# Kernel tuning notes

Hardware: AMD Instinct MI355X
Metric: run time of the kernel (lower is better)

## Reference

```python
import jax, jax.numpy as jnp
import numpy as np

WS = 8        # window_size
SHIFT = 4     # shift_size
NH = 6        # num_heads
EPS = 1e-5


def _rel_pos_index(ws):
    coords = np.stack(np.meshgrid(np.arange(ws), np.arange(ws), indexing='ij'))  # [2,ws,ws]
    cf = coords.reshape(2, -1)                      # [2, ws*ws]
    rel = cf[:, :, None] - cf[:, None, :]           # [2, N, N]
    rel = rel.transpose(1, 2, 0)                    # [N, N, 2]
    rel[:, :, 0] += ws - 1
    rel[:, :, 1] += ws - 1
    rel[:, :, 0] *= 2 * ws - 1
    return rel.sum(-1)                              # [N, N] int


def _attn_mask(H, W, ws, shift):
    img = np.zeros((H, W), dtype=np.float32)
    slices = (slice(0, -ws), slice(-ws, -shift), slice(-shift, None))
    cnt = 0
    for hs in slices:
        for wsl in slices:
            img[hs, wsl] = cnt
            cnt += 1
    mw = img.reshape(H // ws, ws, W // ws, ws).transpose(0, 2, 1, 3).reshape(-1, ws * ws)
    diff = mw[:, None, :] - mw[:, :, None]          # [nW, N, N]
    return np.where(diff != 0, -100.0, 0.0).astype(np.float32)


def _layernorm(x, g, b):
    mu = x.mean(-1, keepdims=True)
    var = ((x - mu) ** 2).mean(-1, keepdims=True)
    return (x - mu) * jax.lax.rsqrt(var + EPS) * g + b


def setup_inputs() -> dict:
    key = jax.random.key(0)
    ks = jax.random.split(key, 8)
    C, HID = 192, 768
    return {
        'x': jax.random.normal(ks[0], (8, 128, 128, C), jnp.float32),
        'g1': jnp.ones((C,), jnp.float32),
        'b1': jnp.zeros((C,), jnp.float32),
        'qkv_w': jax.random.normal(ks[1], (3 * C, C), jnp.float32) * 0.02,
        'qkv_b': jnp.zeros((3 * C,), jnp.float32),
        'rpb_table': jax.random.normal(ks[2], ((2 * WS - 1) ** 2, NH), jnp.float32) * 0.02,
        'proj_w': jax.random.normal(ks[3], (C, C), jnp.float32) * 0.02,
        'proj_b': jnp.zeros((C,), jnp.float32),
        'g2': jnp.ones((C,), jnp.float32),
        'b2': jnp.zeros((C,), jnp.float32),
        'fc1_w': jax.random.normal(ks[4], (HID, C), jnp.float32) * 0.02,
        'fc1_b': jnp.zeros((HID,), jnp.float32),
        'fc2_w': jax.random.normal(ks[5], (C, HID), jnp.float32) * 0.02,
        'fc2_b': jnp.zeros((C,), jnp.float32),
    }


def reference(x, g1, b1, qkv_w, qkv_b, rpb_table, proj_w, proj_b, g2, b2,
              fc1_w, fc1_b, fc2_w, fc2_b):
    B, H, W, C = x.shape
    N = WS * WS
    hd = C // NH
    scale = hd ** -0.5

    rpi = jnp.asarray(_rel_pos_index(WS))                 # [N,N] static
    mask = jnp.asarray(_attn_mask(H, W, WS, SHIFT))       # [nW,N,N] static
    nW = mask.shape[0]

    shortcut = x.reshape(B, H * W, C)
    xn = _layernorm(shortcut, g1, b1).reshape(B, H, W, C)

    # cyclic shift
    xs = jnp.roll(xn, shift=(-SHIFT, -SHIFT), axis=(1, 2))

    # window partition -> [B*nW, N, C]
    win = xs.reshape(B, H // WS, WS, W // WS, WS, C).transpose(0, 1, 3, 2, 4, 5)
    win = win.reshape(-1, N, C)
    B_ = win.shape[0]

    # qkv
    qkv = jnp.einsum('bnc,oc->bno', win, qkv_w) + qkv_b   # [B_,N,3C]
    qkv = qkv.reshape(B_, N, 3, NH, hd).transpose(2, 0, 3, 1, 4)  # [3,B_,NH,N,hd]
    q, k, v = qkv[0] * scale, qkv[1], qkv[2]

    attn = jnp.einsum('bhnd,bhmd->bhnm', q, k)            # [B_,NH,N,N]
    bias = rpb_table[rpi.reshape(-1)].reshape(N, N, NH).transpose(2, 0, 1)
    attn = attn + bias[None]
    attn = attn.reshape(B, nW, NH, N, N) + mask[None, :, None]
    attn = jax.nn.softmax(attn.reshape(B_, NH, N, N), axis=-1)

    out = jnp.einsum('bhnm,bhmd->bhnd', attn, v)          # [B_,NH,N,hd]
    out = out.transpose(0, 2, 1, 3).reshape(B_, N, C)
    out = jnp.einsum('bnc,oc->bno', out, proj_w) + proj_b

    # window reverse -> [B,H,W,C]
    out = out.reshape(B, H // WS, W // WS, WS, WS, C).transpose(0, 1, 3, 2, 4, 5)
    out = out.reshape(B, H, W, C)
    out = jnp.roll(out, shift=(SHIFT, SHIFT), axis=(1, 2)).reshape(B, H * W, C)

    x1 = shortcut + out
    h = _layernorm(x1, g2, b2)
    h = jnp.einsum('bnc,hc->bnh', h, fc1_w) + fc1_b
    h = jax.nn.gelu(h, approximate=False)
    h = jnp.einsum('bnh,ch->bnc', h, fc2_w) + fc2_b
    x2 = x1 + h
    return x2.reshape(B, H, W, C)
```

## Files before the change

kernel.cpp:

```cpp
#include <hip/hip_runtime.h>
#include <hip/hip_bf16.h>

typedef __attribute__((ext_vector_type(8))) short s16x8;
typedef __attribute__((ext_vector_type(4))) float f32x4;

__device__ __forceinline__ unsigned short f2bf(float f){
    __hip_bfloat16 h = __float2bfloat16(f);
    return *reinterpret_cast<unsigned short*>(&h);
}

__device__ __forceinline__ int flab(int g){ return (g < 120) ? 0 : ((g < 124) ? 1 : 2); }

__device__ __forceinline__ void async16(const void* g, void* l){
    __builtin_amdgcn_global_load_lds(
        (const __attribute__((address_space(1))) unsigned int*)g,
        (__attribute__((address_space(3))) unsigned int*)l, 16, 0, 0);
}

__global__ __launch_bounds__(256) void wconv_all(
    const float* __restrict__ w0, const float* __restrict__ w1,
    const float* __restrict__ w2, const float* __restrict__ w3,
    unsigned short* __restrict__ o0, unsigned short* __restrict__ o1,
    unsigned short* __restrict__ o2, unsigned short* __restrict__ o3)
{
    int i = blockIdx.x*256 + threadIdx.x;
    if (i < 110592) o0[i] = f2bf(w0[i]);
    if (i < 36864)  o1[i] = f2bf(w1[i]);
    if (i < 147456) o2[i] = f2bf(w2[i]);
    if (i < 147456) o3[i] = f2bf(w3[i]);
}

__global__ __launch_bounds__(256) void lnqkv_kernel(
    const float* __restrict__ x, const float* __restrict__ g1, const float* __restrict__ b1,
    const unsigned short* __restrict__ wq, const float* __restrict__ qkvb,
    unsigned short* __restrict__ qo, unsigned short* __restrict__ ko,
    unsigned short* __restrict__ vo)
{
    __shared__ __attribute__((aligned(16))) unsigned short win[64*200];
    __shared__ __attribute__((aligned(16))) unsigned short Bs[64*200];
    const int b_ = blockIdx.x;
    const int bb = b_>>8, wi = b_&255, wh = wi>>4, ww = wi&15;
    const int tid = threadIdx.x;
    const int wv = tid>>6, lane = tid&63, lrow = lane&15, quad = lane>>4;

    {
        const int n = tid>>2, q4 = tid&3;
        const int r = n>>3, c = n&7;
        const int hh = (wh*8 + r + 4)&127, wp = (ww*8 + c + 4)&127;
        const float* px = x + (((size_t)bb*128+hh)*128+wp)*192 + q4*48;
        float v[48];
        #pragma unroll
        for (int m=0;m<12;++m) *(float4*)(v+m*4) = *(const float4*)(px+m*4);
        float s = 0.f;
        #pragma unroll
        for (int k=0;k<48;++k) s += v[k];
        s += __shfl_xor(s,1); s += __shfl_xor(s,2);
        float mu = s*(1.0f/192.0f);
        float qv = 0.f;
        #pragma unroll
        for (int k=0;k<48;++k){ float d=v[k]-mu; qv += d*d; }
        qv += __shfl_xor(qv,1); qv += __shfl_xor(qv,2);
        float rstd = rsqrtf(qv*(1.0f/192.0f) + 1e-5f);
        const float* pg = g1 + q4*48;
        const float* pb = b1 + q4*48;
        unsigned short* pw = win + n*200 + q4*48;
        #pragma unroll
        for (int k=0;k<48;++k) pw[k] = f2bf((v[k]-mu)*rstd*pg[k] + pb[k]);
    }
    __syncthreads();

    s16x8 af[6];
    #pragma unroll
    for (int kc=0;kc<6;++kc)
        af[kc] = *(const s16x8*)(win + (wv*16+lrow)*200 + kc*32 + quad*8);

    for (int ot=0; ot<9; ++ot) {
        const int o0 = ot*64;
        __syncthreads();
        #pragma unroll
        for (int t=0;t<6;++t) {
            int cid = tid + t*256;
            *(int4*)(Bs + (cid/24)*200 + (cid%24)*8) =
                *(const int4*)(wq + (size_t)o0*192 + cid*8);
        }
        __syncthreads();
        f32x4 acc[4];
        #pragma unroll
        for (int j=0;j<4;++j) acc[j] = (f32x4){0.f,0.f,0.f,0.f};
        #pragma unroll
        for (int kc=0;kc<6;++kc)
            #pragma unroll
            for (int j=0;j<4;++j) {
                s16x8 bf = *(const s16x8*)(Bs + (j*16+lrow)*200 + kc*32 + quad*8);
                acc[j] = __builtin_amdgcn_mfma_f32_16x16x32_bf16(af[kc], bf, acc[j], 0, 0, 0);
            }
        __syncthreads();
        unsigned short* T = Bs;
        const int part = ot/3;
        float bv[4];
        #pragma unroll
        for (int j=0;j<4;++j) bv[j] = qkvb[o0 + j*16 + lrow];

        if (part < 2) {
            const float scale = (part==0) ? 0.17677669529663687f : 1.0f;
            #pragma unroll
            for (int j=0;j<4;++j)
                #pragma unroll
                for (int rg=0;rg<4;++rg) {
                    int n2 = wv*16 + quad*4 + rg;
                    T[n2*72 + j*16 + lrow] = f2bf((acc[j][rg]+bv[j])*scale);
                }
            __syncthreads();
            unsigned short* dst = (part==0) ? qo : ko;
            #pragma unroll
            for (int t=0;t<2;++t) {
                int c = tid + t*256;
                int n2 = c>>3, blk = c&7;
                int o_in = o0 + blk*8 - part*192;
                int head = o_in>>5, d = o_in&31;
                *(int4*)(dst + (((size_t)b_*6+head)*64 + n2)*32 + d) =
                    *(const int4*)(T + n2*72 + blk*8);
            }
        } else {
            #pragma unroll
            for (int j=0;j<4;++j)
                #pragma unroll
                for (int rg=0;rg<4;++rg) {
                    int n2 = wv*16 + quad*4 + rg;
                    T[(j*16+lrow)*72 + n2] = f2bf(acc[j][rg]+bv[j]);
                }
            __syncthreads();
            #pragma unroll
            for (int t=0;t<2;++t) {
                int c = tid + t*256;
                int ol = c>>3, nb = (c&7)*8;
                int o_in = o0 + ol - 384;
                int head = o_in>>5, d = o_in&31;
                *(int4*)(vo + (((size_t)b_*6+head)*32 + d)*64 + nb) =
                    *(const int4*)(T + ol*72 + nb);
            }
        }
    }
}

__global__ __launch_bounds__(384) void attn_kernel(
    const unsigned short* __restrict__ q, const unsigned short* __restrict__ k,
    const unsigned short* __restrict__ vT, const float* __restrict__ rpb,
    unsigned short* __restrict__ ao)
{
    __shared__ float rpb_s[1350];
    __shared__ __attribute__((aligned(16))) unsigned short p_lds[6*4608];
    const int b_ = blockIdx.x;
    const int h = threadIdx.x >> 6;
    const int lane = threadIdx.x & 63, lrow = lane & 15, quad = lane >> 4;
    for (int i = threadIdx.x; i < 1350; i += 384) rpb_s[i] = rpb[i];
    __syncthreads();

    const size_t hb = ((size_t)b_*6 + h)*2048;
    const unsigned short* qb = q  + hb;
    const unsigned short* kb = k  + hb;
    const unsigned short* vb = vT + hb;

    s16x8 qf[4], kf[4];
    #pragma unroll
    for (int i = 0; i < 4; ++i) qf[i] = *(const s16x8*)(qb + (i*16+lrow)*32 + quad*8);
    #pragma unroll
    for (int j = 0; j < 4; ++j) kf[j] = *(const s16x8*)(kb + (j*16+lrow)*32 + quad*8);

    const f32x4 zz = {0.f,0.f,0.f,0.f};
    f32x4 s[4][4];
    #pragma unroll
    for (int i = 0; i < 4; ++i)
        #pragma unroll
        for (int j = 0; j < 4; ++j)
            s[i][j] = __builtin_amdgcn_mfma_f32_16x16x32_bf16(qf[i], kf[j], zz, 0, 0, 0);

    const int wi = b_ & 255, wh = wi >> 4, ww = wi & 15;
    int labm[4];
    #pragma unroll
    for (int j = 0; j < 4; ++j) {
        int m = j*16 + lrow;
        labm[j] = flab(wh*8 + (m >> 3))*3 + flab(ww*8 + (m & 7));
    }
    unsigned short* pl = p_lds + h*4608;
    #pragma unroll
    for (int i = 0; i < 4; ++i) {
        #pragma unroll
        for (int rg = 0; rg < 4; ++rg) {
            int n = i*16 + quad*4 + rg;
            int rn = n >> 3, cn = n & 7;
            int labn = flab(wh*8 + rn)*3 + flab(ww*8 + cn);
            float vals[4];
            float vmax = -1e30f;
            #pragma unroll
            for (int j = 0; j < 4; ++j) {
                int m = j*16 + lrow;
                int idx = ((rn - (m >> 3) + 7)*15 + (cn - (m & 7) + 7))*6 + h;
                float val = s[i][j][rg] + rpb_s[idx];
                if (labn != labm[j]) val -= 100.f;
                vals[j] = val;
                vmax = fmaxf(vmax, val);
            }
            #pragma unroll
            for (int o = 1; o < 16; o <<= 1) vmax = fmaxf(vmax, __shfl_xor(vmax, o));
            float sum = 0.f;
            #pragma unroll
            for (int j = 0; j < 4; ++j) { vals[j] = __expf(vals[j] - vmax); sum += vals[j]; }
            #pragma unroll
            for (int o = 1; o < 16; o <<= 1) sum += __shfl_xor(sum, o);
            float inv = 1.f / sum;
            #pragma unroll
            for (int j = 0; j < 4; ++j) pl[n*72 + j*16 + lrow] = f2bf(vals[j]*inv);
        }
    }
    __syncthreads();

    f32x4 oacc[4][2];
    #pragma unroll
    for (int i = 0; i < 4; ++i) { oacc[i][0] = zz; oacc[i][1] = zz; }
    #pragma unroll
    for (int kc = 0; kc < 2; ++kc) {
        s16x8 vf[2];
        #pragma unroll
        for (int jd = 0; jd < 2; ++jd)
            vf[jd] = *(const s16x8*)(vb + (jd*16+lrow)*64 + kc*32 + quad*8);
        #pragma unroll
        for (int i = 0; i < 4; ++i) {
            s16x8 pf = *(const s16x8*)(pl + (i*16+lrow)*72 + kc*32 + quad*8);
            #pragma unroll
            for (int jd = 0; jd < 2; ++jd)
                oacc[i][jd] = __builtin_amdgcn_mfma_f32_16x16x32_bf16(pf, vf[jd], oacc[i][jd], 0, 0, 0);
        }
    }
    unsigned short* ob = ao + (size_t)b_*12288 + h*32;
    #pragma unroll
    for (int i = 0; i < 4; ++i)
        #pragma unroll
        for (int jd = 0; jd < 2; ++jd)
            #pragma unroll
            for (int rg = 0; rg < 4; ++rg) {
                int n = i*16 + quad*4 + rg;
                ob[(size_t)n*192 + jd*16 + lrow] = f2bf(oacc[i][jd][rg]);
            }
}

__device__ __forceinline__ void mm64x192(
    const unsigned short* __restrict__ A, const unsigned short* __restrict__ W,
    size_t m0, unsigned short* As, unsigned short* Bs, f32x4 (&acc)[12])
{
    const int tid = threadIdx.x, wv = tid>>6, lane = tid&63;
    const int lrow = lane&15, quad = lane>>4;
    const int grow = lane>>2;
    const int gcb  = (lane&3) ^ ((lane>>3)&3);
    #pragma unroll
    for (int j=0;j<12;++j) acc[j] = (f32x4){0.f,0.f,0.f,0.f};

    const unsigned short* Ab = A + (m0 + grow)*192 + gcb*8;
    const unsigned short* Wb = W + (size_t)grow*192 + gcb*8;

    auto issue = [&](int k0, unsigned short* Ad, unsigned short* Bd) {
        async16(Ab + (size_t)(wv*16)*192 + k0,     Ad + wv*512);
        async16(Wb + (size_t)(wv*16)*192 + k0,     Bd + wv*512);
        async16(Wb + (size_t)((wv+4)*16)*192 + k0, Bd + (wv+4)*512);
        async16(Wb + (size_t)((wv+8)*16)*192 + k0, Bd + (wv+8)*512);
    };
    issue(0, As, Bs);
    int cur = 0;
    for (int k0=0; k0<192; k0+=32) {
        __syncthreads();
        if (k0+32 < 192) issue(k0+32, As + (cur^1)*2048, Bs + (cur^1)*6144);
        const unsigned short* Ac = As + cur*2048;
        const unsigned short* Bc = Bs + cur*6144;
        const int rs = (quad ^ ((lrow>>1)&3)) << 3;
        s16x8 af = *(const s16x8*)(Ac + (wv*16+lrow)*32 + rs);
        #pragma unroll
        for (int j=0;j<12;++j) {
            s16x8 bf = *(const s16x8*)(Bc + (j*16+lrow)*32 + rs);
            acc[j] = __builtin_amdgcn_mfma_f32_16x16x32_bf16(af, bf, acc[j], 0, 0, 0);
        }
        cur ^= 1;
    }
}

__global__ __launch_bounds__(256) void projln_kernel(
    const unsigned short* __restrict__ A, const unsigned short* __restrict__ W,
    const float* __restrict__ pbias, const float* __restrict__ x,
    const float* __restrict__ g2, const float* __restrict__ b2,
    float* __restrict__ x1, unsigned short* __restrict__ xln2b)
{
    __shared__ __attribute__((aligned(16))) char smem[32768];
    unsigned short* As = (unsigned short*)smem;
    unsigned short* Bs = (unsigned short*)(smem + 8192);
    const int b_ = blockIdx.x;
    const int tid = threadIdx.x, wv = tid>>6, lane = tid&63;
    const int lrow = lane&15, quad = lane>>4;
    const size_t m0 = (size_t)b_*64;

    f32x4 acc[12];
    mm64x192(A, W, m0, As, Bs, acc);
    __syncthreads();

    const int bb = b_>>8, wi = b_&255, wh = wi>>4, ww = wi&15;
    float bv[12], gv[12], b2v[12];
    #pragma unroll
    for (int j=0;j<12;++j) {
        bv[j]  = pbias[j*16+lrow];
        gv[j]  = g2[j*16+lrow];
        b2v[j] = b2[j*16+lrow];
    }
    unsigned short* T = (unsigned short*)smem;
    #pragma unroll
    for (int rg=0;rg<4;++rg) {
        int n2 = wv*16 + quad*4 + rg;
        int r = n2>>3, c = n2&7;
        int hh = (wh*8+r+4)&127, wp = (ww*8+c+4)&127;
        size_t tok = ((size_t)bb*128+hh)*128 + wp;
        float xv[12];
        float s = 0.f;
        #pragma unroll
        for (int j=0;j<12;++j) {
            float t = acc[j][rg] + bv[j] + x[tok*192 + j*16 + lrow];
            xv[j] = t; s += t;
        }
        #pragma unroll
        for (int o=1;o<16;o<<=1) s += __shfl_xor(s, o);
        float mu = s*(1.0f/192.0f);
        float qv = 0.f;
        #pragma unroll
        for (int j=0;j<12;++j){ float d = xv[j]-mu; qv += d*d; }
        #pragma unroll
        for (int o=1;o<16;o<<=1) qv += __shfl_xor(qv, o);
        float rstd = rsqrtf(qv*(1.0f/192.0f) + 1e-5f);
        #pragma unroll
        for (int j=0;j<12;++j) {
            x1[tok*192 + j*16 + lrow] = xv[j];
            T[n2*200 + j*16 + lrow] = f2bf((xv[j]-mu)*rstd*gv[j] + b2v[j]);
        }
    }
    __syncthreads();
    #pragma unroll
    for (int t=0;t<6;++t) {
        int cid = tid + t*256;
        int n2 = cid/24, blk = cid%24;
        int r = n2>>3, c = n2&7;
        int hh = (wh*8+r+4)&127, wp = (ww*8+c+4)&127;
        size_t tok = ((size_t)bb*128+hh)*128 + wp;
        int row = (int)(tok & 127);
        int ks = blk>>2, kb = blk&3;
        int sw = (kb ^ ((row>>1)&3)) << 3;
        *(int4*)(xln2b + (tok>>7)*24576 + ks*4096 + row*32 + sw) =
            *(const int4*)(T + n2*200 + blk*8);
    }
}

__global__ __launch_bounds__(256, 4) void gemm_fc1_kernel(
    const unsigned short* __restrict__ Ablk, const unsigned short* __restrict__ Wm,
    const float* __restrict__ bias, unsigned short* __restrict__ h1b)
{
    __shared__ __attribute__((aligned(16))) char smem[28672];
    unsigned short* As = (unsigned short*)smem;
    unsigned short* Bs = (unsigned short*)(smem + 16384);
    const int bid = blockIdx.x;
    const int virt = (bid & 7)*1024 + (bid >> 3);
    const int mt = virt >> 3;
    const int o0 = (virt & 7)*96;
    const int tid = threadIdx.x, wv = tid>>6, lane = tid&63;
    const int lrow = lane&15, quad = lane>>4;
    const int grow = lane>>2, gcb = (lane&3)^((lane>>3)&3);

    const unsigned short* Asrc = Ablk + (size_t)mt*24576 + lane*8;
    const unsigned short* Wb = Wm + (size_t)(o0 + grow)*192 + gcb*8;

    f32x4 acc[2][6];
    #pragma unroll
    for (int i=0;i<2;++i)
        #pragma unroll
        for (int j=0;j<6;++j) acc[i][j] = (f32x4){0.f,0.f,0.f,0.f};

    auto issue = [&](int ks, unsigned short* Ad, unsigned short* Bd) {
        async16(Asrc + ks*4096 + wv*512,     Ad + wv*512);
        async16(Asrc + ks*4096 + (wv+4)*512, Ad + (wv+4)*512);
        async16(Wb + (size_t)(wv*16)*192 + ks*32, Bd + wv*512);
        if (wv < 2)
            async16(Wb + (size_t)((wv+4)*16)*192 + ks*32, Bd + (wv+4)*512);
    };
    issue(0, As, Bs);
    int cur = 0;
    for (int ks=0; ks<6; ++ks) {
        __syncthreads();
        if (ks < 5) issue(ks+1, As + (cur^1)*4096, Bs + (cur^1)*3072);
        const unsigned short* Ac = As + cur*4096;
        const unsigned short* Bc = Bs + cur*3072;
        const int rs = (quad ^ ((lrow>>1)&3)) << 3;
        s16x8 af[2], bf[6];
        #pragma unroll
        for (int i=0;i<2;++i)
            af[i] = *(const s16x8*)(Ac + (wv*32 + i*16 + lrow)*32 + rs);
        #pragma unroll
        for (int j=0;j<6;++j)
            bf[j] = *(const s16x8*)(Bc + (j*16 + lrow)*32 + rs);
        #pragma unroll
        for (int i=0;i<2;++i)
            #pragma unroll
            for (int j=0;j<6;++j)
                acc[i][j] = __builtin_amdgcn_mfma_f32_16x16x32_bf16(af[i], bf[j], acc[i][j], 0, 0, 0);
        cur ^= 1;
    }

    float bv[6];
    #pragma unroll
    for (int j=0;j<6;++j) bv[j] = bias[o0 + j*16 + lrow];
    __syncthreads();
    unsigned short* T = (unsigned short*)smem;
    #pragma unroll
    for (int i=0;i<2;++i)
        #pragma unroll
        for (int j=0;j<6;++j)
            #pragma unroll
            for (int rg=0;rg<4;++rg) {
                int ml = wv*32 + i*16 + quad*4 + rg;
                float v = acc[i][j][rg] + bv[j];
                float v2 = v*v;
                float z = v*(1.5957691216057308f + 0.07135481627f*v2);
                float r = v * __builtin_amdgcn_rcpf(1.f + __expf(-z));
                T[ml*104 + j*16 + lrow] = f2bf(r);
            }
    __syncthreads();
    unsigned short* hb = h1b + (size_t)mt*98304 + (o0>>5)*4096;
    #pragma unroll
    for (int t=0;t<6;++t) {
        int c = tid + t*256;
        int row = c/12, blk = c%12;
        int ks = blk>>2, kb = blk&3;
        int sw = (kb ^ ((row>>1)&3)) << 3;
        *(int4*)(hb + ks*4096 + row*32 + sw) = *(const int4*)(T + row*104 + blk*8);
    }
}

__global__ __launch_bounds__(256, 3) void gemm_fc2_kernel(
    const unsigned short* __restrict__ Ablk, const unsigned short* __restrict__ Wm,
    const float* __restrict__ bias, const float* __restrict__ x1, float* __restrict__ out)
{
    __shared__ __attribute__((aligned(16))) char smem[40960];
    unsigned short* As = (unsigned short*)smem;
    unsigned short* Bs = (unsigned short*)(smem + 16384);
    const int bid = blockIdx.x;
    const int virt = (bid & 7)*128 + (bid >> 3);
    const size_t m0 = (size_t)virt*128;
    const int tid = threadIdx.x, wv = tid>>6, lane = tid&63;
    const int lrow = lane&15, quad = lane>>4;
    const int grow = lane>>2, gcb = (lane&3)^((lane>>3)&3);

    const unsigned short* Asrc = Ablk + (size_t)virt*98304 + lane*8;
    const unsigned short* Wb = Wm + (size_t)grow*768 + gcb*8;

    f32x4 acc[2][12];
    #pragma unroll
    for (int i=0;i<2;++i)
        #pragma unroll
        for (int j=0;j<12;++j) acc[i][j] = (f32x4){0.f,0.f,0.f,0.f};

    auto issue = [&](int ks, unsigned short* Ad, unsigned short* Bd) {
        async16(Asrc + ks*4096 + wv*512,     Ad + wv*512);
        async16(Asrc + ks*4096 + (wv+4)*512, Ad + (wv+4)*512);
        #pragma unroll
        for (int it=0;it<3;++it) {
            int seg = wv + it*4;
            async16(Wb + (size_t)(seg*16)*768 + ks*32, Bd + seg*512);
        }
    };
    issue(0, As, Bs);
    int cur = 0;
    for (int ks=0; ks<24; ++ks) {
        __syncthreads();
        if (ks < 23) issue(ks+1, As + (cur^1)*4096, Bs + (cur^1)*6144);
        const unsigned short* Ac = As + cur*4096;
        const unsigned short* Bc = Bs + cur*6144;
        const int rs = (quad ^ ((lrow>>1)&3)) << 3;
        s16x8 af[2], bf[12];
        #pragma unroll
        for (int i=0;i<2;++i)
            af[i] = *(const s16x8*)(Ac + (wv*32 + i*16 + lrow)*32 + rs);
        #pragma unroll
        for (int j=0;j<12;++j)
            bf[j] = *(const s16x8*)(Bc + (j*16 + lrow)*32 + rs);
        #pragma unroll
        for (int i=0;i<2;++i)
            #pragma unroll
            for (int j=0;j<12;++j)
                acc[i][j] = __builtin_amdgcn_mfma_f32_16x16x32_bf16(af[i], bf[j], acc[i][j], 0, 0, 0);
        cur ^= 1;
    }

    float bv[12];
    #pragma unroll
    for (int j=0;j<12;++j) bv[j] = bias[j*16 + lrow];
    #pragma unroll
    for (int i=0;i<2;++i)
        #pragma unroll
        for (int j=0;j<12;++j)
            #pragma unroll
            for (int rg=0;rg<4;++rg) {
                size_t ad = (m0 + wv*32 + i*16 + quad*4 + rg)*192 + j*16 + lrow;
                out[ad] = acc[i][j][rg] + bv[j] + x1[ad];
            }
}

extern "C" void kernel_launch(void* const* d_in, const int* in_sizes, int n_in,
                              void* d_out, int out_size, void* d_ws, size_t ws_size,
                              hipStream_t stream)
{
    const float* x      = (const float*)d_in[0];
    const float* g1     = (const float*)d_in[1];
    const float* b1     = (const float*)d_in[2];
    const float* qkv_w  = (const float*)d_in[3];
    const float* qkv_b  = (const float*)d_in[4];
    const float* rpb    = (const float*)d_in[5];
    const float* proj_w = (const float*)d_in[6];
    const float* proj_b = (const float*)d_in[7];
    const float* g2     = (const float*)d_in[8];
    const float* b2     = (const float*)d_in[9];
    const float* fc1_w  = (const float*)d_in[10];
    const float* fc1_b  = (const float*)d_in[11];
    const float* fc2_w  = (const float*)d_in[12];
    const float* fc2_b  = (const float*)d_in[13];
    float* out = (float*)d_out;
    char* ws = (char*)d_ws;

    if (ws_size < 353206272ULL) return;

    unsigned short* qbuf  = (unsigned short*)(ws + 0);
    unsigned short* kbuf  = (unsigned short*)(ws + 50331648);
    unsigned short* vbuf  = (unsigned short*)(ws + 100663296);
    unsigned short* attnO = (unsigned short*)(ws + 150994944);
    float*          x1    = (float*)        (ws + 201326592);
    unsigned short* xln2  = (unsigned short*)(ws + 301989888);
    unsigned short* wq    = (unsigned short*)(ws + 352321536);
    unsigned short* wp    = (unsigned short*)(ws + 352321536 + 221184);
    unsigned short* w1    = (unsigned short*)(ws + 352321536 + 221184 + 73728);
    unsigned short* w2    = (unsigned short*)(ws + 352321536 + 221184 + 73728 + 294912);
    unsigned short* h1    = (unsigned short*)(ws + 0);

    wconv_all<<<576, 256, 0, stream>>>(qkv_w, proj_w, fc1_w, fc2_w, wq, wp, w1, w2);
    lnqkv_kernel<<<2048, 256, 0, stream>>>(x, g1, b1, wq, qkv_b, qbuf, kbuf, vbuf);
    attn_kernel<<<2048, 384, 0, stream>>>(qbuf, kbuf, vbuf, rpb, attnO);
    projln_kernel<<<2048, 256, 0, stream>>>(attnO, wp, proj_b, x, g2, b2, x1, xln2);
    gemm_fc1_kernel<<<8192, 256, 0, stream>>>(xln2, w1, fc1_b, h1);
    gemm_fc2_kernel<<<1024, 256, 0, stream>>>(h1, w2, fc2_b, x1, out);
}
```

Before: 575.6 us.

## Fuse fc1, GELU and fc2 into one MLP kernel keeping hidden activations in LDS

Replaces the separate fc1 and fc2 GEMM kernels with a single kernel in which each 512-thread block handles 64 tokens. The block computes fc1 plus GELU into a 96 KB LDS buffer and then runs fc2 from LDS, so the 768-wide hidden tensor never makes a round trip through global memory. The weight conversion now writes fc1/fc2 weights in a pre-tiled blocked layout so B fragments can be read straight from global memory (L2) without LDS staging. The trade-offs are the large LDS footprint, which limits occupancy, and weight reads that are now unpipelined global loads inside the MFMA loops.

```diff
diff --git a/kernel.cpp b/kernel.cpp
--- a/kernel.cpp
+++ b/kernel.cpp
@@ -26,8 +26,16 @@
     int i = blockIdx.x*256 + threadIdx.x;
     if (i < 110592) o0[i] = f2bf(w0[i]);
     if (i < 36864)  o1[i] = f2bf(w1[i]);
-    if (i < 147456) o2[i] = f2bf(w2[i]);
-    if (i < 147456) o3[i] = f2bf(w3[i]);
+    if (i < 147456) {
+        int o = i/192, k = i - o*192;
+        int oc = o/96, r = o - oc*96, ks = k>>5, c = k&31;
+        o2[((oc*6 + ks)*96 + r)*32 + c] = f2bf(w2[i]);
+    }
+    if (i < 147456) {
+        int o = i/768, k = i - o*768;
+        int q = o/48, r = o - q*48, ks = k>>5, c = k&31;
+        o3[((q*24 + ks)*48 + r)*32 + c] = f2bf(w3[i]);
+    }
 }
 
 __global__ __launch_bounds__(256) void lnqkv_kernel(
@@ -353,157 +361,112 @@
     }
 }
 
-__global__ __launch_bounds__(256, 4) void gemm_fc1_kernel(
-    const unsigned short* __restrict__ Ablk, const unsigned short* __restrict__ Wm,
-    const float* __restrict__ bias, unsigned short* __restrict__ h1b)
-{
-    __shared__ __attribute__((aligned(16))) char smem[28672];
-    unsigned short* As = (unsigned short*)smem;
-    unsigned short* Bs = (unsigned short*)(smem + 16384);
-    const int bid = blockIdx.x;
-    const int virt = (bid & 7)*1024 + (bid >> 3);
-    const int mt = virt >> 3;
-    const int o0 = (virt & 7)*96;
+__global__ __launch_bounds__(512, 2) void mlp_kernel(
+    const unsigned short* __restrict__ Ablk,
+    const unsigned short* __restrict__ W1b,
+    const float* __restrict__ fc1b,
+    const unsigned short* __restrict__ W2b,
+    const float* __restrict__ fc2b,
+    const float* __restrict__ x1, float* __restrict__ out)
+{
+    __shared__ __attribute__((aligned(16))) unsigned short Ald[6*2048];
+    __shared__ __attribute__((aligned(16))) unsigned short Hld[24*2048];
+    const int b_ = blockIdx.x;
+    const int mt = b_>>1, half = b_&1;
     const int tid = threadIdx.x, wv = tid>>6, lane = tid&63;
     const int lrow = lane&15, quad = lane>>4;
-    const int grow = lane>>2, gcb = (lane&3)^((lane>>3)&3);
-
-    const unsigned short* Asrc = Ablk + (size_t)mt*24576 + lane*8;
-    const unsigned short* Wb = Wm + (size_t)(o0 + grow)*192 + gcb*8;
-
-    f32x4 acc[2][6];
-    #pragma unroll
-    for (int i=0;i<2;++i)
+    const int rs = (quad ^ ((lrow>>1)&3)) << 3;
+
+    {
+        const unsigned short* src = Ablk + (size_t)mt*24576 + half*2048 + lane*8;
+        #pragma unroll
+        for (int r=0;r<3;++r) {
+            int c = r*8 + wv;
+            async16(src + (c>>2)*4096 + (c&3)*512, Ald + c*512);
+        }
+    }
+    __syncthreads();
+
+    f32x4 acc[4][6];
+    #pragma unroll
+    for (int i=0;i<4;++i)
         #pragma unroll
         for (int j=0;j<6;++j) acc[i][j] = (f32x4){0.f,0.f,0.f,0.f};
-
-    auto issue = [&](int ks, unsigned short* Ad, unsigned short* Bd) {
-        async16(Asrc + ks*4096 + wv*512,     Ad + wv*512);
-        async16(Asrc + ks*4096 + (wv+4)*512, Ad + (wv+4)*512);
-        async16(Wb + (size_t)(wv*16)*192 + ks*32, Bd + wv*512);
-        if (wv < 2)
-            async16(Wb + (size_t)((wv+4)*16)*192 + ks*32, Bd + (wv+4)*512);
-    };
-    issue(0, As, Bs);
-    int cur = 0;
-    for (int ks=0; ks<6; ++ks) {
-        __syncthreads();
-        if (ks < 5) issue(ks+1, As + (cur^1)*4096, Bs + (cur^1)*3072);
-        const unsigned short* Ac = As + cur*4096;
-        const unsigned short* Bc = Bs + cur*3072;
-        const int rs = (quad ^ ((lrow>>1)&3)) << 3;
-        s16x8 af[2], bf[6];
-        #pragma unroll
-        for (int i=0;i<2;++i)
-            af[i] = *(const s16x8*)(Ac + (wv*32 + i*16 + lrow)*32 + rs);
+    #pragma unroll 2
+    for (int ks=0;ks<6;++ks) {
+        s16x8 af[4], bf[6];
+        #pragma unroll
+        for (int i=0;i<4;++i)
+            af[i] = *(const s16x8*)(Ald + ks*2048 + (i*16+lrow)*32 + rs);
         #pragma unroll
         for (int j=0;j<6;++j)
-            bf[j] = *(const s16x8*)(Bc + (j*16 + lrow)*32 + rs);
-        #pragma unroll
-        for (int i=0;i<2;++i)
+            bf[j] = *(const s16x8*)(W1b + (size_t)((wv*6+ks)*96 + j*16+lrow)*32 + quad*8);
+        #pragma unroll
+        for (int i=0;i<4;++i)
             #pragma unroll
             for (int j=0;j<6;++j)
                 acc[i][j] = __builtin_amdgcn_mfma_f32_16x16x32_bf16(af[i], bf[j], acc[i][j], 0, 0, 0);
-        cur ^= 1;
-    }
-
-    float bv[6];
-    #pragma unroll
-    for (int j=0;j<6;++j) bv[j] = bias[o0 + j*16 + lrow];
-    __syncthreads();
-    unsigned short* T = (unsigned short*)smem;
+    }
+
+    {
+        float bv1[6];
+        #pragma unroll
+        for (int j=0;j<6;++j) bv1[j] = fc1b[wv*96 + j*16 + lrow];
+        #pragma unroll
+        for (int i=0;i<4;++i)
+            #pragma unroll
+            for (int j=0;j<6;++j)
+                #pragma unroll
+                for (int rg=0;rg<4;++rg) {
+                    int row = i*16 + quad*4 + rg;
+                    int o = wv*96 + j*16 + lrow;
+                    float v = acc[i][j][rg] + bv1[j];
+                    float v2 = v*v;
+                    float z = v*(1.5957691216057308f + 0.07135481627f*v2);
+                    float r = v * __builtin_amdgcn_rcpf(1.f + __expf(-z));
+                    int ksh = o>>5, c5 = o&31;
+                    Hld[ksh*2048 + row*32 + (((c5>>3) ^ ((row>>1)&3))<<3) + (c5&7)] = f2bf(r);
+                }
+    }
+    __syncthreads();
+
+    const int r0 = (wv>>2)*32, c0 = (wv&3)*48;
+    f32x4 a2[2][3];
     #pragma unroll
     for (int i=0;i<2;++i)
         #pragma unroll
-        for (int j=0;j<6;++j)
-            #pragma unroll
-            for (int rg=0;rg<4;++rg) {
-                int ml = wv*32 + i*16 + quad*4 + rg;
-                float v = acc[i][j][rg] + bv[j];
-                float v2 = v*v;
-                float z = v*(1.5957691216057308f + 0.07135481627f*v2);
-                float r = v * __builtin_amdgcn_rcpf(1.f + __expf(-z));
-                T[ml*104 + j*16 + lrow] = f2bf(r);
-            }
-    __syncthreads();
-    unsigned short* hb = h1b + (size_t)mt*98304 + (o0>>5)*4096;
-    #pragma unroll
-    for (int t=0;t<6;++t) {
-        int c = tid + t*256;
-        int row = c/12, blk = c%12;
-        int ks = blk>>2, kb = blk&3;
-        int sw = (kb ^ ((row>>1)&3)) << 3;
-        *(int4*)(hb + ks*4096 + row*32 + sw) = *(const int4*)(T + row*104 + blk*8);
-    }
-}
-
-__global__ __launch_bounds__(256, 3) void gemm_fc2_kernel(
-    const unsigned short* __restrict__ Ablk, const unsigned short* __restrict__ Wm,
-    const float* __restrict__ bias, const float* __restrict__ x1, float* __restrict__ out)
-{
-    __shared__ __attribute__((aligned(16))) char smem[40960];
-    unsigned short* As = (unsigned short*)smem;
-    unsigned short* Bs = (unsigned short*)(smem + 16384);
-    const int bid = blockIdx.x;
-    const int virt = (bid & 7)*128 + (bid >> 3);
-    const size_t m0 = (size_t)virt*128;
-    const int tid = threadIdx.x, wv = tid>>6, lane = tid&63;
-    const int lrow = lane&15, quad = lane>>4;
-    const int grow = lane>>2, gcb = (lane&3)^((lane>>3)&3);
-
-    const unsigned short* Asrc = Ablk + (size_t)virt*98304 + lane*8;
-    const unsigned short* Wb = Wm + (size_t)grow*768 + gcb*8;
-
-    f32x4 acc[2][12];
-    #pragma unroll
-    for (int i=0;i<2;++i)
-        #pragma unroll
-        for (int j=0;j<12;++j) acc[i][j] = (f32x4){0.f,0.f,0.f,0.f};
-
-    auto issue = [&](int ks, unsigned short* Ad, unsigned short* Bd) {
-        async16(Asrc + ks*4096 + wv*512,     Ad + wv*512);
-        async16(Asrc + ks*4096 + (wv+4)*512, Ad + (wv+4)*512);
-        #pragma unroll
-        for (int it=0;it<3;++it) {
-            int seg = wv + it*4;
-            async16(Wb + (size_t)(seg*16)*768 + ks*32, Bd + seg*512);
-        }
-    };
-    issue(0, As, Bs);
-    int cur = 0;
-    for (int ks=0; ks<24; ++ks) {
-        __syncthreads();
-        if (ks < 23) issue(ks+1, As + (cur^1)*4096, Bs + (cur^1)*6144);
-        const unsigned short* Ac = As + cur*4096;
-        const unsigned short* Bc = Bs + cur*6144;
-        const int rs = (quad ^ ((lrow>>1)&3)) << 3;
-        s16x8 af[2], bf[12];
+        for (int j=0;j<3;++j) a2[i][j] = (f32x4){0.f,0.f,0.f,0.f};
+    #pragma unroll 4
+    for (int ks=0;ks<24;++ks) {
+        s16x8 af2[2], bf2[3];
         #pragma unroll
         for (int i=0;i<2;++i)
-            af[i] = *(const s16x8*)(Ac + (wv*32 + i*16 + lrow)*32 + rs);
-        #pragma unroll
-        for (int j=0;j<12;++j)
-            bf[j] = *(const s16x8*)(Bc + (j*16 + lrow)*32 + rs);
+            af2[i] = *(const s16x8*)(Hld + ks*2048 + (r0 + i*16 + lrow)*32 + rs);
+        #pragma unroll
+        for (int j=0;j<3;++j)
+            bf2[j] = *(const s16x8*)(W2b + (size_t)(((wv&3)*24 + ks)*48 + j*16+lrow)*32 + quad*8);
         #pragma unroll
         for (int i=0;i<2;++i)
             #pragma unroll
-            for (int j=0;j<12;++j)
-                acc[i][j] = __builtin_amdgcn_mfma_f32_16x16x32_bf16(af[i], bf[j], acc[i][j], 0, 0, 0);
-        cur ^= 1;
-    }
-
-    float bv[12];
-    #pragma unroll
-    for (int j=0;j<12;++j) bv[j] = bias[j*16 + lrow];
-    #pragma unroll
-    for (int i=0;i<2;++i)
-        #pragma unroll
-        for (int j=0;j<12;++j)
-            #pragma unroll
-            for (int rg=0;rg<4;++rg) {
-                size_t ad = (m0 + wv*32 + i*16 + quad*4 + rg)*192 + j*16 + lrow;
-                out[ad] = acc[i][j][rg] + bv[j] + x1[ad];
-            }
+            for (int j=0;j<3;++j)
+                a2[i][j] = __builtin_amdgcn_mfma_f32_16x16x32_bf16(af2[i], bf2[j], a2[i][j], 0, 0, 0);
+    }
+
+    {
+        float bv2[3];
+        #pragma unroll
+        for (int j=0;j<3;++j) bv2[j] = fc2b[c0 + j*16 + lrow];
+        #pragma unroll
+        for (int i=0;i<2;++i)
+            #pragma unroll
+            for (int j=0;j<3;++j)
+                #pragma unroll
+                for (int rg=0;rg<4;++rg) {
+                    size_t grow = (size_t)mt*128 + half*64 + r0 + i*16 + quad*4 + rg;
+                    size_t ad = grow*192 + c0 + j*16 + lrow;
+                    out[ad] = a2[i][j][rg] + bv2[j] + x1[ad];
+                }
+    }
 }
 
 extern "C" void kernel_launch(void* const* d_in, const int* in_sizes, int n_in,
@@ -537,14 +500,12 @@
     unsigned short* xln2  = (unsigned short*)(ws + 301989888);
     unsigned short* wq    = (unsigned short*)(ws + 352321536);
     unsigned short* wp    = (unsigned short*)(ws + 352321536 + 221184);
-    unsigned short* w1    = (unsigned short*)(ws + 352321536 + 221184 + 73728);
-    unsigned short* w2    = (unsigned short*)(ws + 352321536 + 221184 + 73728 + 294912);
-    unsigned short* h1    = (unsigned short*)(ws + 0);
-
-    wconv_all<<<576, 256, 0, stream>>>(qkv_w, proj_w, fc1_w, fc2_w, wq, wp, w1, w2);
+    unsigned short* w1b   = (unsigned short*)(ws + 352321536 + 221184 + 73728);
+    unsigned short* w2b   = (unsigned short*)(ws + 352321536 + 221184 + 73728 + 294912);
+
+    wconv_all<<<576, 256, 0, stream>>>(qkv_w, proj_w, fc1_w, fc2_w, wq, wp, w1b, w2b);
     lnqkv_kernel<<<2048, 256, 0, stream>>>(x, g1, b1, wq, qkv_b, qbuf, kbuf, vbuf);
     attn_kernel<<<2048, 384, 0, stream>>>(qbuf, kbuf, vbuf, rpb, attnO);
     projln_kernel<<<2048, 256, 0, stream>>>(attnO, wp, proj_b, x, g2, b2, x1, xln2);
-    gemm_fc1_kernel<<<8192, 256, 0, stream>>>(xln2, w1, fc1_b, h1);
-    gemm_fc2_kernel<<<1024, 256, 0, stream>>>(h1, w2, fc2_b, x1, out);
-}
+    mlp_kernel<<<2048, 512, 0, stream>>>(xln2, w1b, fc1_b, w2b, fc2_b, x1, out);
+}
```

Result: no change. 581.7 us (+1.1%).
